# Kernel tuning notes

Measured on AMD Instinct MI355X. Metric: run time of the kernel, lower is better.

The kernel has to match this reference:

```python
import jax, jax.numpy as jnp
import numpy as np

V = 32          # number_variables
DEG = 12        # degree
ORDER = 3       # spline_order (cubic)
N_BASIS = DEG + ORDER - 1  # 14, rows of params
LO, HI = -15.0, 15.0       # polynomial_range[:, 0]
EPS = 1e-6


def make_knots():
    dist = (HI - LO) / (DEG - 1)
    k = DEG + 2 * ORDER
    return jnp.linspace(LO - ORDER * dist, HI + ORDER * dist, k, dtype=jnp.float32)


def bspline_basis(x, knots, order):
    # x: [N, P] -> basis: [N, P, N_BASIS] via Cox-de Boor recursion (Naive_Basis)
    xk = x[..., None]
    b = ((xk >= knots[:-1]) & (xk < knots[1:])).astype(x.dtype)  # degree-0, [N,P,K-1]
    t = knots
    for k in range(1, order + 1):
        left = (xk - t[:-(k + 1)]) / (t[k:-1] - t[:-(k + 1)])
        right = (t[k + 1:] - xk) / (t[k + 1:] - t[1:-k])
        b = left * b[..., :-1] + right * b[..., 1:]
    return b  # [N, P, K-1-order] == [N, P, N_BASIS]


def setup_inputs() -> dict:
    key = jax.random.key(0)
    k1, k2 = jax.random.split(key)
    num_lambdas = V * (V - 1) // 2  # 496
    inp = jax.random.normal(k1, (16384, V), dtype=jnp.float32)
    log_d = jnp.zeros((16384, V), dtype=jnp.float32)
    params = 0.001 * jnp.ones((N_BASIS, num_lambdas), dtype=jnp.float32)
    return {"input": inp, "log_d": log_d, "params": params}


def reference(input, log_d, params):
    n = input.shape[0]
    knots = make_knots()
    rows, cols = np.tril_indices(V, -1)  # matches torch.tril_indices(V, V, offset=-1)
    rows = jnp.asarray(rows); cols = jnp.asarray(cols)
    # clamp into half-open spline support for valid degree-0 basis
    x = jnp.clip(input, LO, HI - EPS)
    xs = x[:, cols]                                  # [N, P] per-pair covariate values
    basis = bspline_basis(xs, knots, ORDER)          # [N, P, N_BASIS]
    lam = jnp.einsum('npk,kp->np', basis, params)    # [N, P] lambda values
    # lower-triangular lambda matrix: identity + strict lower entries
    lm = jnp.broadcast_to(jnp.eye(V, dtype=input.dtype), (n, V, V))
    lm = lm.at[:, rows, cols].set(lam)
    out = jnp.einsum('nvc,nc->nv', lm, input)        # bmm(lambda_matrix, input)
    # ridge penalties on spline coefficients (penalize_towards=0)
    d2 = jnp.diff(params, n=2, axis=0)
    d1 = jnp.diff(params, n=1, axis=0)
    second_pen = jnp.sum(d2 ** 2)
    first_pen = jnp.sum(d1 ** 2)
    param_pen = jnp.sum(params ** 2)
    return out, lm, second_pen, first_pen, param_pen
```

## Files before the change

kernel.cpp:

```cpp
#include <hip/hip_runtime.h>

#define VDIM   32
#define NPAIR  496
#define NBASIS 14
#define NPARAM (NBASIS * NPAIR)
#define ROWS   16

typedef float f32x4 __attribute__((ext_vector_type(4)));

__global__ __launch_bounds__(256) void Decorrelation_35270271435435_kernel(
    const float* __restrict__ input,
    const float* __restrict__ params,
    float* __restrict__ out,
    float* __restrict__ lm,
    float* __restrict__ pens,
    int N)
{
    __shared__ float sp[NPARAM];
    __shared__ float xin[ROWS][VDIM];
    __shared__ float wgt[4][ROWS][VDIM];
    __shared__ int   ib [ROWS][VDIM];

    const int tid = threadIdx.x;
    const int n0  = blockIdx.x * ROWS;

    {
        const f32x4* p4 = (const f32x4*)params;
        f32x4*       s4 = (f32x4*)sp;
        for (int i = tid; i < NPARAM / 4; i += 256) s4[i] = p4[i];
    }

    #pragma unroll
    for (int it = 0; it < 2; ++it) {
        const int item = tid + it * 256;
        const int r = item >> 5, c = item & 31;
        const int n = n0 + r;
        const float xi = (n < N) ? input[n * VDIM + c] : 0.0f;
        xin[r][c] = xi;
        const float dist = 30.0f / 11.0f;
        const float invd = 11.0f / 30.0f;
        const float t0   = -15.0f - 3.0f * dist;
        float x = fminf(fmaxf(xi, -15.0f), 15.0f - 1e-6f);
        float u = (x - t0) * invd;
        int   i = (int)floorf(u);
        i = min(13, max(3, i));
        const float uu  = u - (float)i;
        const float om  = 1.0f - uu;
        const float uu2 = uu * uu, uu3 = uu2 * uu;
        const float sixth = 1.0f / 6.0f;
        wgt[0][r][c] = om * om * om * sixth;
        wgt[1][r][c] = (3.0f * uu3 - 6.0f * uu2 + 4.0f) * sixth;
        wgt[2][r][c] = (-3.0f * uu3 + 3.0f * uu2 + 3.0f * uu + 1.0f) * sixth;
        wgt[3][r][c] = uu3 * sixth;
        ib[r][c] = (i - 3) * NPAIR;
    }
    __syncthreads();

    const int v  = tid >> 3;
    const int c0 = (tid & 7) << 2;
    int  pidx[4];
    bool low[4], dia[4];
    #pragma unroll
    for (int j = 0; j < 4; ++j) {
        const int c = c0 + j;
        low[j]  = (c < v);
        dia[j]  = (c == v);
        pidx[j] = (v * (v - 1)) / 2 + c;
    }

    float* lmp = lm + (size_t)n0 * (VDIM * VDIM) + tid * 4;

    for (int r = 0; r < ROWS; ++r, lmp += VDIM * VDIM) {
        const int n = n0 + r;
        if (n >= N) break;
        float vals[4];
        float partial = 0.0f;
        #pragma unroll
        for (int j = 0; j < 4; ++j) {
            const int c = c0 + j;
            float val;
            if (dia[j]) {
                val = 1.0f;
            } else if (low[j]) {
                const int b = ib[r][c] + pidx[j];
                val = wgt[0][r][c] * sp[b]
                    + wgt[1][r][c] * sp[b + NPAIR]
                    + wgt[2][r][c] * sp[b + 2 * NPAIR]
                    + wgt[3][r][c] * sp[b + 3 * NPAIR];
            } else {
                val = 0.0f;
            }
            vals[j] = val;
            partial += val * xin[r][c];
        }
        f32x4 f4 = { vals[0], vals[1], vals[2], vals[3] };
        __builtin_nontemporal_store(f4, (f32x4*)lmp);

        partial += __shfl_down(partial, 4, 8);
        partial += __shfl_down(partial, 2, 8);
        partial += __shfl_down(partial, 1, 8);
        if ((tid & 7) == 0) out[n * VDIM + v] = partial;
    }

    if (blockIdx.x == 0) {
        float s2 = 0.0f, s1 = 0.0f, spn = 0.0f;
        for (int idx = tid; idx < NPARAM; idx += 256) {
            const float a = sp[idx];
            spn += a * a;
            if (idx < NPARAM - NPAIR) {
                const float b = sp[idx + NPAIR];
                const float d1 = b - a;
                s1 += d1 * d1;
                if (idx < NPARAM - 2 * NPAIR) {
                    const float c = sp[idx + 2 * NPAIR];
                    const float d2 = c - 2.0f * b + a;
                    s2 += d2 * d2;
                }
            }
        }
        #pragma unroll
        for (int off = 32; off > 0; off >>= 1) {
            s2  += __shfl_down(s2, off);
            s1  += __shfl_down(s1, off);
            spn += __shfl_down(spn, off);
        }
        __shared__ float wsum[3][4];
        const int lane = tid & 63, wid = tid >> 6;
        if (lane == 0) { wsum[0][wid] = s2; wsum[1][wid] = s1; wsum[2][wid] = spn; }
        __syncthreads();
        if (tid == 0) {
            pens[0] = wsum[0][0] + wsum[0][1] + wsum[0][2] + wsum[0][3];
            pens[1] = wsum[1][0] + wsum[1][1] + wsum[1][2] + wsum[1][3];
            pens[2] = wsum[2][0] + wsum[2][1] + wsum[2][2] + wsum[2][3];
        }
    }
}

extern "C" void kernel_launch(void* const* d_in, const int* in_sizes, int n_in,
                              void* d_out, int out_size, void* d_ws, size_t ws_size,
                              hipStream_t stream) {
    const float* input  = (const float*)d_in[0];
    const float* params = (const float*)d_in[2];
    const int N = in_sizes[0] / VDIM;

    float* out  = (float*)d_out;
    float* lm   = out + (size_t)N * VDIM;
    float* pens = lm + (size_t)N * VDIM * VDIM;

    const int nb = (N + ROWS - 1) / ROWS;
    Decorrelation_35270271435435_kernel<<<nb, 256, 0, stream>>>(
        input, params, out, lm, pens, N);
}
```

Measured before the change: 93.99 us.

## Prepack spline params into per-pair interval vectors and drop per-block LDS param copy

Adds a one-block prep kernel that repacks params into f32x4 windows per pair and interval in the workspace, and moves the penalty sums into that kernel. The main kernel no longer copies the full 27 KB parameter table into LDS in every block. It computes each pair's lambda once per row with a single vector gather from global memory, stores the results in a padded LDS lambda buffer, then emits the lm rows from it. This removes the redundant per-block parameter staging and the scattered LDS reads, at the cost of an extra kernel launch and gathers that rely on L2.

```diff
diff --git a/kernel.cpp b/kernel.cpp
--- a/kernel.cpp
+++ b/kernel.cpp
@@ -4,31 +4,80 @@
 #define NPAIR  496
 #define NBASIS 14
 #define NPARAM (NBASIS * NPAIR)
+#define NINT   11
 #define ROWS   16
+#define LROW   544
 
 typedef float f32x4 __attribute__((ext_vector_type(4)));
 
+__device__ __forceinline__ int seg_of(int v) {
+    int m = v - 1;
+    if (m <= 0) return 0;
+    int q = m >> 2, r = m & 3;
+    return 4 * (2 * q * (q + 1) + r * (q + 1));
+}
+
+__global__ __launch_bounds__(256) void Decorrelation_prep(
+    const float* __restrict__ params,
+    f32x4* __restrict__ ptv,
+    float* __restrict__ pens)
+{
+    const int tid = threadIdx.x;
+    for (int i = 0; i < NINT; ++i) {
+        for (int p = tid; p < NPAIR; p += 256) {
+            f32x4 w = { params[(i    ) * NPAIR + p],
+                        params[(i + 1) * NPAIR + p],
+                        params[(i + 2) * NPAIR + p],
+                        params[(i + 3) * NPAIR + p] };
+            ptv[p * NINT + i] = w;
+        }
+    }
+    float s2 = 0.f, s1 = 0.f, sp = 0.f;
+    for (int idx = tid; idx < NPARAM; idx += 256) {
+        const float a = params[idx];
+        sp += a * a;
+        if (idx < NPARAM - NPAIR) {
+            const float b = params[idx + NPAIR];
+            const float d1 = b - a;
+            s1 += d1 * d1;
+            if (idx < NPARAM - 2 * NPAIR) {
+                const float c = params[idx + 2 * NPAIR];
+                const float d2 = c - 2.f * b + a;
+                s2 += d2 * d2;
+            }
+        }
+    }
+    #pragma unroll
+    for (int off = 32; off > 0; off >>= 1) {
+        s2 += __shfl_down(s2, off);
+        s1 += __shfl_down(s1, off);
+        sp += __shfl_down(sp, off);
+    }
+    __shared__ float ws[3][4];
+    const int lane = tid & 63, wid = tid >> 6;
+    if (lane == 0) { ws[0][wid] = s2; ws[1][wid] = s1; ws[2][wid] = sp; }
+    __syncthreads();
+    if (tid == 0) {
+        pens[0] = ws[0][0] + ws[0][1] + ws[0][2] + ws[0][3];
+        pens[1] = ws[1][0] + ws[1][1] + ws[1][2] + ws[1][3];
+        pens[2] = ws[2][0] + ws[2][1] + ws[2][2] + ws[2][3];
+    }
+}
+
 __global__ __launch_bounds__(256) void Decorrelation_35270271435435_kernel(
     const float* __restrict__ input,
-    const float* __restrict__ params,
+    const f32x4* __restrict__ ptv,
     float* __restrict__ out,
     float* __restrict__ lm,
-    float* __restrict__ pens,
     int N)
 {
-    __shared__ float sp[NPARAM];
-    __shared__ float xin[ROWS][VDIM];
-    __shared__ float wgt[4][ROWS][VDIM];
-    __shared__ int   ib [ROWS][VDIM];
+    __shared__ f32x4 wgt4[ROWS][VDIM];
+    __shared__ float xin [ROWS][VDIM];
+    __shared__ int   ibk [ROWS][VDIM];
+    __shared__ float lam [ROWS][LROW];
 
     const int tid = threadIdx.x;
     const int n0  = blockIdx.x * ROWS;
-
-    {
-        const f32x4* p4 = (const f32x4*)params;
-        f32x4*       s4 = (f32x4*)sp;
-        for (int i = tid; i < NPARAM / 4; i += 256) s4[i] = p4[i];
-    }
 
     #pragma unroll
     for (int it = 0; it < 2; ++it) {
@@ -48,50 +97,69 @@
         const float om  = 1.0f - uu;
         const float uu2 = uu * uu, uu3 = uu2 * uu;
         const float sixth = 1.0f / 6.0f;
-        wgt[0][r][c] = om * om * om * sixth;
-        wgt[1][r][c] = (3.0f * uu3 - 6.0f * uu2 + 4.0f) * sixth;
-        wgt[2][r][c] = (-3.0f * uu3 + 3.0f * uu2 + 3.0f * uu + 1.0f) * sixth;
-        wgt[3][r][c] = uu3 * sixth;
-        ib[r][c] = (i - 3) * NPAIR;
+        f32x4 w = { om * om * om * sixth,
+                    (3.0f * uu3 - 6.0f * uu2 + 4.0f) * sixth,
+                    (-3.0f * uu3 + 3.0f * uu2 + 3.0f * uu + 1.0f) * sixth,
+                    uu3 * sixth };
+        wgt4[r][c] = w;
+        ibk[r][c]  = i - 3;
+    }
+
+    const int p1 = tid;
+    int v1 = (int)((1.0f + sqrtf(8.0f * (float)p1 + 1.0f)) * 0.5f);
+    while (v1 * (v1 - 1) / 2 > p1) --v1;
+    while ((v1 + 1) * v1 / 2 <= p1) ++v1;
+    const int c1 = p1 - v1 * (v1 - 1) / 2;
+    const int o1 = seg_of(v1) + c1;
+
+    const int  p2   = tid + 256;
+    const bool has2 = (p2 < NPAIR);
+    int v2 = 1, c2 = 0, o2 = 0;
+    if (has2) {
+        v2 = (int)((1.0f + sqrtf(8.0f * (float)p2 + 1.0f)) * 0.5f);
+        while (v2 * (v2 - 1) / 2 > p2) --v2;
+        while ((v2 + 1) * v2 / 2 <= p2) ++v2;
+        c2 = p2 - v2 * (v2 - 1) / 2;
+        o2 = seg_of(v2) + c2;
     }
     __syncthreads();
 
-    const int v  = tid >> 3;
-    const int c0 = (tid & 7) << 2;
-    int  pidx[4];
-    bool low[4], dia[4];
-    #pragma unroll
-    for (int j = 0; j < 4; ++j) {
-        const int c = c0 + j;
-        low[j]  = (c < v);
-        dia[j]  = (c == v);
-        pidx[j] = (v * (v - 1)) / 2 + c;
+    #pragma unroll 4
+    for (int r = 0; r < ROWS; ++r) {
+        {
+            const f32x4 w = wgt4[r][c1];
+            const f32x4 q = ptv[p1 * NINT + ibk[r][c1]];
+            lam[r][o1] = w.x * q.x + w.y * q.y + w.z * q.z + w.w * q.w;
+        }
+        if (has2) {
+            const f32x4 w = wgt4[r][c2];
+            const f32x4 q = ptv[p2 * NINT + ibk[r][c2]];
+            lam[r][o2] = w.x * q.x + w.y * q.y + w.z * q.z + w.w * q.w;
+        }
     }
+    __syncthreads();
 
+    const int v    = tid >> 3;
+    const int c0   = (tid & 7) << 2;
+    const int segv = seg_of(v);
     float* lmp = lm + (size_t)n0 * (VDIM * VDIM) + tid * 4;
 
+    #pragma unroll 4
     for (int r = 0; r < ROWS; ++r, lmp += VDIM * VDIM) {
         const int n = n0 + r;
         if (n >= N) break;
+        const f32x4 lq = *(const f32x4*)&lam[r][segv + c0];
+        const f32x4 xq = *(const f32x4*)&xin[r][c0];
         float vals[4];
         float partial = 0.0f;
         #pragma unroll
         for (int j = 0; j < 4; ++j) {
             const int c = c0 + j;
-            float val;
-            if (dia[j]) {
-                val = 1.0f;
-            } else if (low[j]) {
-                const int b = ib[r][c] + pidx[j];
-                val = wgt[0][r][c] * sp[b]
-                    + wgt[1][r][c] * sp[b + NPAIR]
-                    + wgt[2][r][c] * sp[b + 2 * NPAIR]
-                    + wgt[3][r][c] * sp[b + 3 * NPAIR];
-            } else {
-                val = 0.0f;
-            }
+            const float lv = (j == 0) ? lq.x : (j == 1) ? lq.y : (j == 2) ? lq.z : lq.w;
+            const float xv = (j == 0) ? xq.x : (j == 1) ? xq.y : (j == 2) ? xq.z : xq.w;
+            const float val = (c < v) ? lv : ((c == v) ? 1.0f : 0.0f);
             vals[j] = val;
-            partial += val * xin[r][c];
+            partial += val * xv;
         }
         f32x4 f4 = { vals[0], vals[1], vals[2], vals[3] };
         __builtin_nontemporal_store(f4, (f32x4*)lmp);
@@ -100,39 +168,6 @@
         partial += __shfl_down(partial, 2, 8);
         partial += __shfl_down(partial, 1, 8);
         if ((tid & 7) == 0) out[n * VDIM + v] = partial;
-    }
-
-    if (blockIdx.x == 0) {
-        float s2 = 0.0f, s1 = 0.0f, spn = 0.0f;
-        for (int idx = tid; idx < NPARAM; idx += 256) {
-            const float a = sp[idx];
-            spn += a * a;
-            if (idx < NPARAM - NPAIR) {
-                const float b = sp[idx + NPAIR];
-                const float d1 = b - a;
-                s1 += d1 * d1;
-                if (idx < NPARAM - 2 * NPAIR) {
-                    const float c = sp[idx + 2 * NPAIR];
-                    const float d2 = c - 2.0f * b + a;
-                    s2 += d2 * d2;
-                }
-            }
-        }
-        #pragma unroll
-        for (int off = 32; off > 0; off >>= 1) {
-            s2  += __shfl_down(s2, off);
-            s1  += __shfl_down(s1, off);
-            spn += __shfl_down(spn, off);
-        }
-        __shared__ float wsum[3][4];
-        const int lane = tid & 63, wid = tid >> 6;
-        if (lane == 0) { wsum[0][wid] = s2; wsum[1][wid] = s1; wsum[2][wid] = spn; }
-        __syncthreads();
-        if (tid == 0) {
-            pens[0] = wsum[0][0] + wsum[0][1] + wsum[0][2] + wsum[0][3];
-            pens[1] = wsum[1][0] + wsum[1][1] + wsum[1][2] + wsum[1][3];
-            pens[2] = wsum[2][0] + wsum[2][1] + wsum[2][2] + wsum[2][3];
-        }
     }
 }
 
@@ -147,7 +182,11 @@
     float* lm   = out + (size_t)N * VDIM;
     float* pens = lm + (size_t)N * VDIM * VDIM;
 
+    f32x4* ptv = (f32x4*)d_ws;
+
+    Decorrelation_prep<<<1, 256, 0, stream>>>(params, ptv, pens);
+
     const int nb = (N + ROWS - 1) / ROWS;
     Decorrelation_35270271435435_kernel<<<nb, 256, 0, stream>>>(
-        input, params, out, lm, pens, N);
+        input, ptv, out, lm, N);
 }
```

Measured after the change: 127.7 us. 35.9% more time.
